# Performance work log

Hardware: AMD Instinct MI355X
Metric: run time of the kernel (lower is better)

Reference implementation:

```python
import jax, jax.numpy as jnp
import numpy as np

N, E = 50000, 800000
IN_DIM, H_DIM, OUT_DIM, EDGE_DIM, HEADS = 128, 128, 112, 8, 1
NEG_SLOPE = 0.2
BN_EPS = 1e-5


def _gat_layer(x, src, dst, edge_att, W, a_src, a_dst, We, a_edge, bias):
    """PyG GATConv (concat=False, edge_dim used for attention only)."""
    H, C = a_src.shape  # heads, out channels
    xs = (x @ W).reshape(-1, H, C)            # [N,H,C]
    ef = (edge_att @ We).reshape(-1, H, C)    # [E,H,C]
    al_src = jnp.einsum('nhc,hc->nh', xs, a_src)   # [N,H]
    al_dst = jnp.einsum('nhc,hc->nh', xs, a_dst)   # [N,H]
    al_edge = jnp.einsum('ehc,hc->eh', ef, a_edge) # [E,H]
    alpha = al_src[src] + al_dst[dst] + al_edge    # [E,H]
    alpha = jnp.where(alpha > 0, alpha, NEG_SLOPE * alpha)  # leaky_relu(0.2)
    # segment softmax over incoming edges of each dst node
    m = jax.lax.stop_gradient(jax.ops.segment_max(alpha, dst, num_segments=N))
    ex = jnp.exp(alpha - m[dst])
    den = jax.ops.segment_sum(ex, dst, num_segments=N)
    att = ex / den[dst]                       # [E,H]
    msg = xs[src] * att[:, :, None]           # [E,H,C] gather + weight
    out = jax.ops.segment_sum(msg, dst, num_segments=N)  # scatter-add [N,H,C]
    return out.mean(axis=1) + bias            # concat=False -> head mean


def _batchnorm(h, gamma, beta):
    mu = h.mean(axis=0)
    var = h.var(axis=0)
    return gamma * (h - mu) * jax.lax.rsqrt(var + BN_EPS) + beta


def setup_inputs() -> dict:
    key = jax.random.key(0)
    ks = jax.random.split(key, 20)
    s = 0.1
    inp = {
        'x': jax.random.normal(ks[0], (N, IN_DIM), dtype=jnp.float32),
        'edge_index': jax.random.randint(ks[1], (2, E), 0, N, dtype=jnp.int32),
        'edge_att': jax.random.normal(ks[2], (E, EDGE_DIM), dtype=jnp.float32),
        # layer 0: IN_DIM -> H_DIM
        'W0': s * jax.random.normal(ks[3], (IN_DIM, HEADS * H_DIM), dtype=jnp.float32),
        'a_src0': s * jax.random.normal(ks[4], (HEADS, H_DIM), dtype=jnp.float32),
        'a_dst0': s * jax.random.normal(ks[5], (HEADS, H_DIM), dtype=jnp.float32),
        'We0': s * jax.random.normal(ks[6], (EDGE_DIM, HEADS * H_DIM), dtype=jnp.float32),
        'a_edge0': s * jax.random.normal(ks[7], (HEADS, H_DIM), dtype=jnp.float32),
        'b0': jnp.zeros((H_DIM,), dtype=jnp.float32),
        # layer 1: H_DIM -> OUT_DIM
        'W1': s * jax.random.normal(ks[8], (H_DIM, HEADS * OUT_DIM), dtype=jnp.float32),
        'a_src1': s * jax.random.normal(ks[9], (HEADS, OUT_DIM), dtype=jnp.float32),
        'a_dst1': s * jax.random.normal(ks[10], (HEADS, OUT_DIM), dtype=jnp.float32),
        'We1': s * jax.random.normal(ks[11], (EDGE_DIM, HEADS * OUT_DIM), dtype=jnp.float32),
        'a_edge1': s * jax.random.normal(ks[12], (HEADS, OUT_DIM), dtype=jnp.float32),
        'b1': jnp.zeros((OUT_DIM,), dtype=jnp.float32),
        # batchnorms
        'bn_g': jnp.ones((H_DIM,), dtype=jnp.float32),
        'bn_b': jnp.zeros((H_DIM,), dtype=jnp.float32),
        'bnf_g': jnp.ones((OUT_DIM,), dtype=jnp.float32),
        'bnf_b': jnp.zeros((OUT_DIM,), dtype=jnp.float32),
    }
    return inp


def reference(x, edge_index, edge_att,
              W0, a_src0, a_dst0, We0, a_edge0, b0,
              W1, a_src1, a_dst1, We1, a_edge1, b1,
              bn_g, bn_b, bnf_g, bnf_b):
    src, dst = edge_index[0], edge_index[1]
    h = _gat_layer(x, src, dst, edge_att, W0, a_src0, a_dst0, We0, a_edge0, b0)
    h = _batchnorm(h, bn_g, bn_b)
    h = jax.nn.relu(h)
    # dropout is a no-op in eval; omitted for a deterministic reference
    h = _gat_layer(h, src, dst, edge_att, W1, a_src1, a_dst1, We1, a_edge1, b1)
    h = _batchnorm(h, bnf_g, bnf_b)
    return h
```

## Files before the change

kernel.cpp:

```cpp
#include <hip/hip_runtime.h>
#include <math.h>

#define NN 50000
#define NPAD 50048
#define NE 800000
#define SCAN_B 256
#define SCAN_NBLK ((NN + SCAN_B - 1) / SCAN_B)
#define AGG_NBLK 3200

typedef __attribute__((ext_vector_type(8))) short bf16x8;
typedef __attribute__((ext_vector_type(4))) float f32x4;
typedef __attribute__((ext_vector_type(8))) unsigned short u16x8;

__device__ __forceinline__ unsigned short f2bf(float x) {
    unsigned u = __float_as_uint(x);
    u += 0x7fffu + ((u >> 16) & 1);
    return (unsigned short)(u >> 16);
}
__device__ __forceinline__ float bf2f(unsigned short h) {
    return __uint_as_float(((unsigned)h) << 16);
}

template<int LAYER>
__device__ __forceinline__ float edge_ex(uint2 r, float aldv, const float* __restrict__ als)
{
    float ae = bf2f((unsigned short)(LAYER ? (r.y & 0xffffu) : (r.x >> 16)));
    float a = als[r.x & 0xffffu] + aldv + ae;
    a = a > 0.f ? a : 0.2f * a;
    return __expf(a);
}

__global__ void k_init_cvt(int* __restrict__ deg, float* __restrict__ stats,
                           int* __restrict__ hist, int* __restrict__ binCur,
                           const float* __restrict__ We0, const float* __restrict__ ae0,
                           const float* __restrict__ We1, const float* __restrict__ ae1,
                           float* __restrict__ ve,
                           const float* __restrict__ W0, const float* __restrict__ W1,
                           unsigned short* __restrict__ Wth0, unsigned short* __restrict__ Wtl0,
                           unsigned short* __restrict__ Wth1, unsigned short* __restrict__ Wtl1)
{
    int idx = blockIdx.x * 256 + threadIdx.x;
    if (idx < NN) deg[idx] = 0;
    if (idx < 512) stats[idx] = 0.f;
    if (idx < 64) { hist[idx] = 0; binCur[idx] = 0; }
    if (idx < 128 * 128) {
        int k = idx / 128, c = idx % 128;
        float v = W0[idx];
        unsigned short hi = f2bf(v);
        Wth0[c * 128 + k] = hi;
        Wtl0[c * 128 + k] = f2bf(v - bf2f(hi));
    } else if (idx < 128 * 128 + 128 * 112) {
        int i2 = idx - 128 * 128;
        int k = i2 / 112, c = i2 % 112;
        float v = W1[i2];
        unsigned short hi = f2bf(v);
        Wth1[c * 128 + k] = hi;
        Wtl1[c * 128 + k] = f2bf(v - bf2f(hi));
    }
    if (blockIdx.x == gridDim.x - 1) {
        int j = threadIdx.x;
        if (j < 8) {
            float s = 0.f;
            for (int c = 0; c < 128; ++c) s += We0[j * 128 + c] * ae0[c];
            ve[j] = s;
        } else if (j < 16) {
            int jj = j - 8;
            float s = 0.f;
            for (int c = 0; c < 112; ++c) s += We1[jj * 112 + c] * ae1[c];
            ve[8 + jj] = s;
        }
    }
}

__global__ void k_deg(const int* __restrict__ dst, int* __restrict__ deg,
                      int* __restrict__ rank, int E_)
{
    int i = blockIdx.x * blockDim.x + threadIdx.x;
    int e = i * 2;
    if (e + 2 <= E_) {
        int2 dd = *reinterpret_cast<const int2*>(dst + e);
        int2 rr;
        rr.x = atomicAdd(&deg[dd.x], 1);
        rr.y = atomicAdd(&deg[dd.y], 1);
        *reinterpret_cast<int2*>(rank + e) = rr;
    } else if (e < E_) {
        rank[e] = atomicAdd(&deg[dst[e]], 1);
    }
}

__global__ void k_scan1(const int* __restrict__ deg, int* __restrict__ partial,
                        int* __restrict__ hist)
{
    __shared__ int sm[SCAN_B];
    __shared__ int lh[64];
    int t = threadIdx.x;
    if (t < 64) lh[t] = 0;
    int idx = blockIdx.x * SCAN_B + t;
    int d = (idx < NN) ? deg[idx] : 0;
    sm[t] = d;
    __syncthreads();
    if (idx < NN) atomicAdd(&lh[63 - (d < 63 ? d : 63)], 1);
    #pragma unroll
    for (int off = SCAN_B / 2; off > 0; off >>= 1) {
        if (t < off) sm[t] += sm[t + off];
        __syncthreads();
    }
    if (t == 0) partial[blockIdx.x] = sm[0];
    if (t < 64 && lh[t]) atomicAdd(&hist[t], lh[t]);
}

__global__ void k_scan3(const int* __restrict__ deg, const int* __restrict__ partial,
                        int* __restrict__ rp, const int* __restrict__ hist,
                        int* __restrict__ binCur, int* __restrict__ ord)
{
    __shared__ int sm[SCAN_B];
    __shared__ int pbase;
    __shared__ int lh[64], lrsv[64], lstart[64];
    int t = threadIdx.x;
    int pv = (t < SCAN_NBLK && t < blockIdx.x) ? partial[t] : 0;
    sm[t] = pv;
    __syncthreads();
    #pragma unroll
    for (int off = SCAN_B / 2; off > 0; off >>= 1) {
        if (t < off) sm[t] += sm[t + off];
        __syncthreads();
    }
    if (t == 0) pbase = sm[0];
    __syncthreads();
    int idx = blockIdx.x * SCAN_B + t;
    int v = (idx < NN) ? deg[idx] : 0;
    sm[t] = v;
    __syncthreads();
    #pragma unroll
    for (int off = 1; off < SCAN_B; off <<= 1) {
        int u = (t >= off) ? sm[t - off] : 0;
        __syncthreads();
        sm[t] += u;
        __syncthreads();
    }
    int excl = pbase + ((t == 0) ? 0 : sm[t - 1]);
    if (idx < NN) rp[idx] = excl;
    if (idx == NN - 1) rp[NN] = excl + v;

    if (t < 64) lh[t] = 0;
    __syncthreads();
    int b = 0, lr = 0;
    if (idx < NN) {
        b = 63 - (v < 63 ? v : 63);
        lr = atomicAdd(&lh[b], 1);
    }
    __syncthreads();
    if (t < 64) {
        lrsv[t] = lh[t] ? atomicAdd(&binCur[t], lh[t]) : 0;
        int s = 0;
        for (int i = 0; i < t; ++i) s += hist[i];
        lstart[t] = s;
    }
    __syncthreads();
    if (idx < NN) ord[lstart[b] + lrsv[b] + lr] = idx;
}

__global__ void k_csr_fill(const int* __restrict__ src, const int* __restrict__ dst,
                           const float* __restrict__ eatt, const float* __restrict__ ve,
                           const int* __restrict__ rp, const int* __restrict__ rank,
                           uint2* __restrict__ pk, int E_)
{
    int i = blockIdx.x * blockDim.x + threadIdx.x;
    int e = i * 4;
    if (e >= E_) return;
    int4 ss = *reinterpret_cast<const int4*>(src + e);
    int4 dd = *reinterpret_cast<const int4*>(dst + e);
    int4 rr = *reinterpret_cast<const int4*>(rank + e);
    const float4* ea = reinterpret_cast<const float4*>(eatt + (size_t)e * 8);

    float v0 = ve[0], v1 = ve[1], v2 = ve[2], v3 = ve[3];
    float v4 = ve[4], v5 = ve[5], v6 = ve[6], v7 = ve[7];
    float w0 = ve[8], w1 = ve[9], w2 = ve[10], w3 = ve[11];
    float w4 = ve[12], w5 = ve[13], w6 = ve[14], w7 = ve[15];

    int s4[4] = {ss.x, ss.y, ss.z, ss.w};
    int d4[4] = {dd.x, dd.y, dd.z, dd.w};
    int r4[4] = {rr.x, rr.y, rr.z, rr.w};
    #pragma unroll
    for (int k = 0; k < 4; ++k) {
        float4 u0 = ea[2 * k], u1 = ea[2 * k + 1];
        float a0 = u0.x * v0 + u0.y * v1 + u0.z * v2 + u0.w * v3
                 + u1.x * v4 + u1.y * v5 + u1.z * v6 + u1.w * v7;
        float a1 = u0.x * w0 + u0.y * w1 + u0.z * w2 + u0.w * w3
                 + u1.x * w4 + u1.y * w5 + u1.z * w6 + u1.w * w7;
        int pos = rp[d4[k]] + r4[k];
        uint2 rec;
        rec.x = (unsigned)s4[k] | ((unsigned)f2bf(a0) << 16);
        rec.y = (unsigned)f2bf(a1);
        pk[pos] = rec;
    }
}

template<int COLS, bool BN_IN>
__launch_bounds__(256, 2)
__global__ void k_gemm_mfma(const void* __restrict__ A,
                            const unsigned short* __restrict__ Wth,
                            const unsigned short* __restrict__ Wtl,
                            unsigned short* __restrict__ out,
                            const float* __restrict__ a_src, const float* __restrict__ a_dst,
                            float* __restrict__ als, float* __restrict__ ald,
                            const float* __restrict__ bsum, const float* __restrict__ bsq,
                            const float* __restrict__ gamma, const float* __restrict__ beta)
{
    constexpr int NT = COLS / 16;
    __shared__ unsigned short sBh[COLS * 128];
    __shared__ unsigned short sBl[COLS * 128];
    __shared__ float scN[128], shN[128];

    int wv = threadIdx.x >> 6;
    int lane = threadIdx.x & 63;
    int r0 = blockIdx.x * 64 + wv * 16;
    int m = lane & 15;
    int quad = lane >> 4;
    int arow = r0 + m;
    int rc = (arow < NN) ? arow : NN - 1;

    float4 av[8];
    u16x8 av16[4];
    if (BN_IN) {
        const unsigned short* pa = reinterpret_cast<const unsigned short*>(A)
                                 + (size_t)rc * 128 + quad * 8;
        #pragma unroll
        for (int ks = 0; ks < 4; ++ks)
            av16[ks] = *reinterpret_cast<const u16x8*>(pa + ks * 32);
    } else {
        const float* pa = reinterpret_cast<const float*>(A) + (size_t)rc * 128 + quad * 8;
        #pragma unroll
        for (int ks = 0; ks < 4; ++ks) {
            av[2 * ks]     = *reinterpret_cast<const float4*>(pa + ks * 32);
            av[2 * ks + 1] = *reinterpret_cast<const float4*>(pa + ks * 32 + 4);
        }
    }

    constexpr int CH = COLS * 128 * 2 / 16;
    for (int i = threadIdx.x; i < CH; i += 256) {
        unsigned o = (unsigned)i * 16u;
        unsigned d = o ^ (((o >> 8) & 7u) << 4);
        *reinterpret_cast<uint4*>(reinterpret_cast<char*>(sBh) + d) =
            *reinterpret_cast<const uint4*>(reinterpret_cast<const char*>(Wth) + o);
        *reinterpret_cast<uint4*>(reinterpret_cast<char*>(sBl) + d) =
            *reinterpret_cast<const uint4*>(reinterpret_cast<const char*>(Wtl) + o);
    }
    if (BN_IN) {
        if (threadIdx.x < 128) {
            int k = threadIdx.x;
            float invn = 1.0f / (float)NN;
            float mean = bsum[k] * invn;
            float var  = bsq[k] * invn - mean * mean;
            float sc = gamma[k] * rsqrtf(var + 1e-5f);
            scN[k] = sc;
            shN[k] = beta[k] - mean * sc;
        }
    }
    __syncthreads();

    f32x4 acc[NT];
    #pragma unroll
    for (int t = 0; t < NT; ++t) acc[t] = f32x4{0.f, 0.f, 0.f, 0.f};

    unsigned swz = ((unsigned)(m & 7)) << 4;

    #pragma unroll
    for (int ks = 0; ks < 4; ++ks) {
        float vv[8];
        if (BN_IN) {
            #pragma unroll
            for (int jj = 0; jj < 8; ++jj) vv[jj] = bf2f((unsigned short)av16[ks][jj]);
        } else {
            float4 v0 = av[2 * ks], v1 = av[2 * ks + 1];
            vv[0] = v0.x; vv[1] = v0.y; vv[2] = v0.z; vv[3] = v0.w;
            vv[4] = v1.x; vv[5] = v1.y; vv[6] = v1.z; vv[7] = v1.w;
        }
        int kb = ks * 32 + quad * 8;
        bf16x8 ah, al;
        #pragma unroll
        for (int jj = 0; jj < 8; ++jj) {
            float f = vv[jj];
            if (BN_IN) f = fmaxf(f * scN[kb + jj] + shN[kb + jj], 0.f);
            unsigned short hi = f2bf(f);
            ah[jj] = (short)hi;
            al[jj] = (short)f2bf(f - bf2f(hi));
        }
        #pragma unroll
        for (int t = 0; t < NT; ++t) {
            int c = t * 16 + m;
            unsigned b = ((unsigned)c * 256u + (unsigned)ks * 64u + (unsigned)quad * 16u) ^ swz;
            bf16x8 bh = *reinterpret_cast<const bf16x8*>(reinterpret_cast<const char*>(sBh) + b);
            bf16x8 bl = *reinterpret_cast<const bf16x8*>(reinterpret_cast<const char*>(sBl) + b);
            acc[t] = __builtin_amdgcn_mfma_f32_16x16x32_bf16(ah, bh, acc[t], 0, 0, 0);
            acc[t] = __builtin_amdgcn_mfma_f32_16x16x32_bf16(al, bh, acc[t], 0, 0, 0);
            acc[t] = __builtin_amdgcn_mfma_f32_16x16x32_bf16(ah, bl, acc[t], 0, 0, 0);
        }
    }

    float p[4] = {0.f, 0.f, 0.f, 0.f}, q[4] = {0.f, 0.f, 0.f, 0.f};
    #pragma unroll
    for (int t = 0; t < NT; ++t) {
        int c = t * 16 + m;
        float asv = a_src[c], adv = a_dst[c];
        #pragma unroll
        for (int rI = 0; rI < 4; ++rI) {
            float v = acc[t][rI];
            int row = r0 + quad * 4 + rI;
            if (row < NN) out[(size_t)row * COLS + c] = f2bf(v);
            p[rI] += v * asv;
            q[rI] += v * adv;
        }
    }
    #pragma unroll
    for (int rI = 0; rI < 4; ++rI) {
        #pragma unroll
        for (int off = 1; off <= 8; off <<= 1) {
            p[rI] += __shfl_xor(p[rI], off);
            q[rI] += __shfl_xor(q[rI], off);
        }
    }
    if (m == 0) {
        #pragma unroll
        for (int rI = 0; rI < 4; ++rI) {
            int row = r0 + quad * 4 + rI;
            if (row < NN) { als[row] = p[rI]; ald[row] = q[rI]; }
        }
    }
}

template<int COLS, int LAYER>
__global__ void k_aggregate(const int* __restrict__ rp, const int* __restrict__ ord,
                            const uint2* __restrict__ pk,
                            const float* __restrict__ als, const float* __restrict__ ald,
                            const unsigned short* __restrict__ xs,
                            unsigned short* __restrict__ out,
                            float* __restrict__ psum, float* __restrict__ psq)
{
    __shared__ float sS[16 * 128], sQ[16 * 128];
    int ql = threadIdx.x & 15;
    int wq = threadIdx.x >> 4;
    int col = ql * 8;
    bool act = (col < COLS);
    int qid = blockIdx.x * 16 + wq;
    float bs[8] = {0.f,0.f,0.f,0.f,0.f,0.f,0.f,0.f};
    float bq[8] = {0.f,0.f,0.f,0.f,0.f,0.f,0.f,0.f};

    if (qid < NN) {
        int w = ord[qid];
        int beg = rp[w], end = rp[w + 1];
        float aldv = ald[w];
        float acc[8] = {0.f,0.f,0.f,0.f,0.f,0.f,0.f,0.f};
        float den = 0.f;
        int j = beg;
        for (; j + 8 <= end; j += 8) {
            uint2 r0 = pk[j],     r1 = pk[j + 1], r2 = pk[j + 2], r3 = pk[j + 3];
            uint2 r4 = pk[j + 4], r5 = pk[j + 5], r6 = pk[j + 6], r7 = pk[j + 7];
            float e0 = edge_ex<LAYER>(r0, aldv, als), e1 = edge_ex<LAYER>(r1, aldv, als);
            float e2 = edge_ex<LAYER>(r2, aldv, als), e3 = edge_ex<LAYER>(r3, aldv, als);
            float e4 = edge_ex<LAYER>(r4, aldv, als), e5 = edge_ex<LAYER>(r5, aldv, als);
            float e6 = edge_ex<LAYER>(r6, aldv, als), e7 = edge_ex<LAYER>(r7, aldv, als);
            den += ((e0 + e1) + (e2 + e3)) + ((e4 + e5) + (e6 + e7));
            if (act) {
                u16x8 u0 = *reinterpret_cast<const u16x8*>(xs + (size_t)(r0.x & 0xffffu) * COLS + col);
                u16x8 u1 = *reinterpret_cast<const u16x8*>(xs + (size_t)(r1.x & 0xffffu) * COLS + col);
                u16x8 u2 = *reinterpret_cast<const u16x8*>(xs + (size_t)(r2.x & 0xffffu) * COLS + col);
                u16x8 u3 = *reinterpret_cast<const u16x8*>(xs + (size_t)(r3.x & 0xffffu) * COLS + col);
                u16x8 u4 = *reinterpret_cast<const u16x8*>(xs + (size_t)(r4.x & 0xffffu) * COLS + col);
                u16x8 u5 = *reinterpret_cast<const u16x8*>(xs + (size_t)(r5.x & 0xffffu) * COLS + col);
                u16x8 u6 = *reinterpret_cast<const u16x8*>(xs + (size_t)(r6.x & 0xffffu) * COLS + col);
                u16x8 u7 = *reinterpret_cast<const u16x8*>(xs + (size_t)(r7.x & 0xffffu) * COLS + col);
                #pragma unroll
                for (int k = 0; k < 8; ++k)
                    acc[k] += (((e0 * bf2f(u0[k]) + e1 * bf2f(u1[k]))
                              + (e2 * bf2f(u2[k]) + e3 * bf2f(u3[k])))
                             + ((e4 * bf2f(u4[k]) + e5 * bf2f(u5[k]))
                              + (e6 * bf2f(u6[k]) + e7 * bf2f(u7[k]))));
            }
        }
        if (j < end) {
            bool v1 = j + 1 < end, v2 = j + 2 < end, v3 = j + 3 < end;
            bool v4 = j + 4 < end, v5 = j + 5 < end, v6 = j + 6 < end;
            uint2 r0 = pk[j];
            uint2 r1 = v1 ? pk[j + 1] : uint2{0u, 0u};
            uint2 r2 = v2 ? pk[j + 2] : uint2{0u, 0u};
            uint2 r3 = v3 ? pk[j + 3] : uint2{0u, 0u};
            uint2 r4 = v4 ? pk[j + 4] : uint2{0u, 0u};
            uint2 r5 = v5 ? pk[j + 5] : uint2{0u, 0u};
            uint2 r6 = v6 ? pk[j + 6] : uint2{0u, 0u};
            float e0 = edge_ex<LAYER>(r0, aldv, als);
            float e1 = v1 ? edge_ex<LAYER>(r1, aldv, als) : 0.f;
            float e2 = v2 ? edge_ex<LAYER>(r2, aldv, als) : 0.f;
            float e3 = v3 ? edge_ex<LAYER>(r3, aldv, als) : 0.f;
            float e4 = v4 ? edge_ex<LAYER>(r4, aldv, als) : 0.f;
            float e5 = v5 ? edge_ex<LAYER>(r5, aldv, als) : 0.f;
            float e6 = v6 ? edge_ex<LAYER>(r6, aldv, als) : 0.f;
            den += ((e0 + e1) + (e2 + e3)) + ((e4 + e5) + e6);
            if (act) {
                u16x8 u0 = *reinterpret_cast<const u16x8*>(xs + (size_t)(r0.x & 0xffffu) * COLS + col);
                #pragma unroll
                for (int k = 0; k < 8; ++k) acc[k] += e0 * bf2f(u0[k]);
                if (v1) {
                    u16x8 u = *reinterpret_cast<const u16x8*>(xs + (size_t)(r1.x & 0xffffu) * COLS + col);
                    #pragma unroll
                    for (int k = 0; k < 8; ++k) acc[k] += e1 * bf2f(u[k]);
                }
                if (v2) {
                    u16x8 u = *reinterpret_cast<const u16x8*>(xs + (size_t)(r2.x & 0xffffu) * COLS + col);
                    #pragma unroll
                    for (int k = 0; k < 8; ++k) acc[k] += e2 * bf2f(u[k]);
                }
                if (v3) {
                    u16x8 u = *reinterpret_cast<const u16x8*>(xs + (size_t)(r3.x & 0xffffu) * COLS + col);
                    #pragma unroll
                    for (int k = 0; k < 8; ++k) acc[k] += e3 * bf2f(u[k]);
                }
                if (v4) {
                    u16x8 u = *reinterpret_cast<const u16x8*>(xs + (size_t)(r4.x & 0xffffu) * COLS + col);
                    #pragma unroll
                    for (int k = 0; k < 8; ++k) acc[k] += e4 * bf2f(u[k]);
                }
                if (v5) {
                    u16x8 u = *reinterpret_cast<const u16x8*>(xs + (size_t)(r5.x & 0xffffu) * COLS + col);
                    #pragma unroll
                    for (int k = 0; k < 8; ++k) acc[k] += e5 * bf2f(u[k]);
                }
                if (v6) {
                    u16x8 u = *reinterpret_cast<const u16x8*>(xs + (size_t)(r6.x & 0xffffu) * COLS + col);
                    #pragma unroll
                    for (int k = 0; k < 8; ++k) acc[k] += e6 * bf2f(u[k]);
                }
            }
        }
        float inv = (end > beg) ? 1.f / den : 0.f;
        if (act) {
            float o[8];
            u16x8 ob;
            #pragma unroll
            for (int k = 0; k < 8; ++k) {
                o[k] = acc[k] * inv;
                bs[k] += o[k];
                bq[k] += o[k] * o[k];
                ob[k] = f2bf(o[k]);
            }
            __builtin_nontemporal_store(ob,
                reinterpret_cast<u16x8*>(out + (size_t)w * COLS + col));
        }
    }
    #pragma unroll
    for (int k = 0; k < 8; ++k) {
        sS[wq * 128 + col + k] = act ? bs[k] : 0.f;
        sQ[wq * 128 + col + k] = act ? bq[k] : 0.f;
    }
    __syncthreads();
    int t = threadIdx.x;
    if (t < 128) {
        float s = 0.f, s2 = 0.f;
        #pragma unroll
        for (int r = 0; r < 16; ++r) { s += sS[r * 128 + t]; s2 += sQ[r * 128 + t]; }
        psum[(size_t)blockIdx.x * 128 + t] = s;
        psq [(size_t)blockIdx.x * 128 + t] = s2;
    }
}

__global__ void k_bn_stats2(const float* __restrict__ psum, const float* __restrict__ psq,
                            float* __restrict__ sums, float* __restrict__ sqs)
{
    int t = threadIdx.x;
    int c = t & 127;
    constexpr int ROWS = AGG_NBLK / 128;
    const float* sp = (t < 128) ? psum : psq;
    float s = 0.f;
    #pragma unroll 5
    for (int i = 0; i < ROWS; ++i)
        s += sp[(size_t)(blockIdx.x * ROWS + i) * 128 + c];
    unsafeAtomicAdd(((t < 128) ? sums : sqs) + c, s);
}

template<int COLS>
__global__ void k_bn_apply(const unsigned short* __restrict__ in, float* __restrict__ out,
                           const float* __restrict__ sums, const float* __restrict__ sqs,
                           const float* __restrict__ gamma, const float* __restrict__ beta,
                           int n)
{
    int idx = blockIdx.x * blockDim.x + threadIdx.x;
    if (idx >= n * COLS) return;
    int c = idx % COLS;
    float invn = 1.0f / (float)n;
    float mean = sums[c] * invn;
    float var  = sqs[c] * invn - mean * mean;
    float sc = gamma[c] * rsqrtf(var + 1e-5f);
    float sh = beta[c] - mean * sc;
    out[idx] = bf2f(in[idx]) * sc + sh;
}

extern "C" void kernel_launch(void* const* d_in, const int* in_sizes, int n_in,
                              void* d_out, int out_size, void* d_ws, size_t ws_size,
                              hipStream_t stream)
{
    const float* x    = (const float*)d_in[0];
    const int*   eidx = (const int*)d_in[1];
    const float* eatt = (const float*)d_in[2];
    const float* W0   = (const float*)d_in[3];
    const float* as0  = (const float*)d_in[4];
    const float* ad0  = (const float*)d_in[5];
    const float* We0  = (const float*)d_in[6];
    const float* ae0  = (const float*)d_in[7];
    const float* W1   = (const float*)d_in[9];
    const float* as1  = (const float*)d_in[10];
    const float* ad1  = (const float*)d_in[11];
    const float* We1  = (const float*)d_in[12];
    const float* ae1  = (const float*)d_in[13];
    const float* bng  = (const float*)d_in[15];
    const float* bnb  = (const float*)d_in[16];
    const float* bnfg = (const float*)d_in[17];
    const float* bnfb = (const float*)d_in[18];

    const int N = NN, E = NE;
    const int* src = eidx;
    const int* dst = eidx + E;

    float* ws = (float*)d_ws;
    size_t off = 0;
    unsigned short* xs0b = (unsigned short*)(ws + off); off += (size_t)N * 64;
    unsigned short* h = (unsigned short*)(ws + off);    off += (size_t)N * 64;
    unsigned short* xs1b = (unsigned short*)(ws + off); off += (size_t)N * 56;
    uint2* pk = (uint2*)(ws + off);     off += (size_t)E * 2;
    int*   rp   = (int*)(ws + off);     off += N + 2;
    int*   ord  = (int*)(ws + off);     off += N;
    float* als0 = ws + off;     off += N;
    float* ald0 = ws + off;     off += N;
    float* als1 = ws + off;     off += N;
    float* ald1 = ws + off;     off += N;
    float* stats = ws + off;    off += 512;
    float* ve = ws + off;       off += 16;
    int*   hist = (int*)(ws + off);     off += 64;
    int*   binCur = (int*)(ws + off);   off += 64;
    int*   partial = (int*)(ws + off);  off += SCAN_NBLK;
    float* psum = ws + off;     off += (size_t)AGG_NBLK * 128;
    float* psq  = ws + off;     off += (size_t)AGG_NBLK * 128;
    unsigned short* Wth0 = (unsigned short*)(ws + off); off += 128 * 64;
    unsigned short* Wtl0 = (unsigned short*)(ws + off); off += 128 * 64;
    unsigned short* Wth1 = (unsigned short*)(ws + off); off += 112 * 64;
    unsigned short* Wtl1 = (unsigned short*)(ws + off); off += 112 * 64;

    int*   rank = (int*)h;
    int*   deg  = ((int*)h) + 800000;
    unsigned short* out1 = h;

    float* sum0 = stats;
    float* sq0  = stats + 128;
    float* sum1 = stats + 256;
    float* sq1  = stats + 384;

    k_init_cvt<<<(N + 255) / 256, 256, 0, stream>>>(deg, stats, hist, binCur,
                                                    We0, ae0, We1, ae1, ve,
                                                    W0, W1, Wth0, Wtl0, Wth1, Wtl1);

    k_deg<<<(E / 2 + 255) / 256, 256, 0, stream>>>(dst, deg, rank, E);
    k_scan1<<<SCAN_NBLK, SCAN_B, 0, stream>>>(deg, partial, hist);
    k_scan3<<<SCAN_NBLK, SCAN_B, 0, stream>>>(deg, partial, rp, hist, binCur, ord);
    k_csr_fill<<<(E / 4 + 255) / 256, 256, 0, stream>>>(src, dst, eatt, ve, rp, rank, pk, E);

    k_gemm_mfma<128, false><<<NPAD / 64, 256, 0, stream>>>(x, Wth0, Wtl0, xs0b,
                                                           as0, ad0, als0, ald0,
                                                           nullptr, nullptr, nullptr, nullptr);
    k_aggregate<128, 0><<<AGG_NBLK, 256, 0, stream>>>(rp, ord, pk, als0, ald0, xs0b, h, psum, psq);
    k_bn_stats2<<<128, 256, 0, stream>>>(psum, psq, sum0, sq0);

    k_gemm_mfma<112, true><<<NPAD / 64, 256, 0, stream>>>(h, Wth1, Wtl1, xs1b,
                                                          as1, ad1, als1, ald1,
                                                          sum0, sq0, bng, bnb);
    k_aggregate<112, 1><<<AGG_NBLK, 256, 0, stream>>>(rp, ord, pk, als1, ald1, xs1b, out1, psum, psq);
    k_bn_stats2<<<128, 256, 0, stream>>>(psum, psq, sum1, sq1);
    k_bn_apply<112><<<(N * 112 + 255) / 256, 256, 0, stream>>>(out1, (float*)d_out, sum1, sq1, bnfg, bnfb, N);
}
```

Before: 329.4 us.

## Build CSR via two-pass bucketed scatter and pack row ranges into order array

Replaces per-edge rank atomics with a coarse bucket scatter (atomic per 49-node bucket) into a temp buffer, followed by a per-bucket local placement pass using shared-memory counters. The node order array now carries row begin/end so aggregation skips separate rp lookups. BN apply is vectorised to four elements per thread. The extra pass and contended bucket counters trade against better write locality and removing the rank array.

```diff
diff --git a/kernel.cpp b/kernel.cpp
--- a/kernel.cpp
+++ b/kernel.cpp
@@ -7,6 +7,8 @@
 #define SCAN_B 256
 #define SCAN_NBLK ((NN + SCAN_B - 1) / SCAN_B)
 #define AGG_NBLK 3200
+#define NBUCK 1024
+#define BWID 49
 
 typedef __attribute__((ext_vector_type(8))) short bf16x8;
 typedef __attribute__((ext_vector_type(4))) float f32x4;
@@ -72,19 +74,18 @@
     }
 }
 
-__global__ void k_deg(const int* __restrict__ dst, int* __restrict__ deg,
-                      int* __restrict__ rank, int E_)
+__global__ void k_deg(const int* __restrict__ dst, int* __restrict__ deg, int E_)
 {
     int i = blockIdx.x * blockDim.x + threadIdx.x;
-    int e = i * 2;
-    if (e + 2 <= E_) {
-        int2 dd = *reinterpret_cast<const int2*>(dst + e);
-        int2 rr;
-        rr.x = atomicAdd(&deg[dd.x], 1);
-        rr.y = atomicAdd(&deg[dd.y], 1);
-        *reinterpret_cast<int2*>(rank + e) = rr;
-    } else if (e < E_) {
-        rank[e] = atomicAdd(&deg[dst[e]], 1);
+    int e = i * 4;
+    if (e + 4 <= E_) {
+        int4 dd = *reinterpret_cast<const int4*>(dst + e);
+        atomicAdd(&deg[dd.x], 1);
+        atomicAdd(&deg[dd.y], 1);
+        atomicAdd(&deg[dd.z], 1);
+        atomicAdd(&deg[dd.w], 1);
+    } else {
+        for (; e < E_; ++e) atomicAdd(&deg[dst[e]], 1);
     }
 }
 
@@ -111,7 +112,7 @@
 
 __global__ void k_scan3(const int* __restrict__ deg, const int* __restrict__ partial,
                         int* __restrict__ rp, const int* __restrict__ hist,
-                        int* __restrict__ binCur, int* __restrict__ ord)
+                        int* __restrict__ binCur, uint4* __restrict__ ordq)
 {
     __shared__ int sm[SCAN_B];
     __shared__ int pbase;
@@ -157,20 +158,34 @@
         lstart[t] = s;
     }
     __syncthreads();
-    if (idx < NN) ord[lstart[b] + lrsv[b] + lr] = idx;
-}
-
-__global__ void k_csr_fill(const int* __restrict__ src, const int* __restrict__ dst,
-                           const float* __restrict__ eatt, const float* __restrict__ ve,
-                           const int* __restrict__ rp, const int* __restrict__ rank,
-                           uint2* __restrict__ pk, int E_)
+    if (idx < NN) {
+        uint4 rec;
+        rec.x = (unsigned)idx;
+        rec.y = (unsigned)excl;
+        rec.z = (unsigned)(excl + v);
+        rec.w = 0u;
+        ordq[lstart[b] + lrsv[b] + lr] = rec;
+    }
+}
+
+__global__ void k_binit(const int* __restrict__ rp, int* __restrict__ bcur)
+{
+    int b = blockIdx.x * blockDim.x + threadIdx.x;
+    if (b < NBUCK) {
+        int nb = b * BWID;
+        bcur[b] = rp[nb < NN ? nb : NN];
+    }
+}
+
+__global__ void k_fill_p1(const int* __restrict__ src, const int* __restrict__ dst,
+                          const float* __restrict__ eatt, const float* __restrict__ ve,
+                          int* __restrict__ bcur, uint2* __restrict__ tmp, int E_)
 {
     int i = blockIdx.x * blockDim.x + threadIdx.x;
     int e = i * 4;
     if (e >= E_) return;
     int4 ss = *reinterpret_cast<const int4*>(src + e);
     int4 dd = *reinterpret_cast<const int4*>(dst + e);
-    int4 rr = *reinterpret_cast<const int4*>(rank + e);
     const float4* ea = reinterpret_cast<const float4*>(eatt + (size_t)e * 8);
 
     float v0 = ve[0], v1 = ve[1], v2 = ve[2], v3 = ve[3];
@@ -180,7 +195,6 @@
 
     int s4[4] = {ss.x, ss.y, ss.z, ss.w};
     int d4[4] = {dd.x, dd.y, dd.z, dd.w};
-    int r4[4] = {rr.x, rr.y, rr.z, rr.w};
     #pragma unroll
     for (int k = 0; k < 4; ++k) {
         float4 u0 = ea[2 * k], u1 = ea[2 * k + 1];
@@ -188,11 +202,36 @@
                  + u1.x * v4 + u1.y * v5 + u1.z * v6 + u1.w * v7;
         float a1 = u0.x * w0 + u0.y * w1 + u0.z * w2 + u0.w * w3
                  + u1.x * w4 + u1.y * w5 + u1.z * w6 + u1.w * w7;
-        int pos = rp[d4[k]] + r4[k];
+        int d = d4[k];
+        int pos = atomicAdd(&bcur[d / BWID], 1);
         uint2 rec;
         rec.x = (unsigned)s4[k] | ((unsigned)f2bf(a0) << 16);
-        rec.y = (unsigned)f2bf(a1);
-        pk[pos] = rec;
+        rec.y = (unsigned)d     | ((unsigned)f2bf(a1) << 16);
+        tmp[pos] = rec;
+    }
+}
+
+__global__ void k_fill_p2(const int* __restrict__ rp, const uint2* __restrict__ tmp,
+                          uint2* __restrict__ pk)
+{
+    __shared__ int lcnt[BWID];
+    int b = blockIdx.x;
+    int t = threadIdx.x;
+    int nb0 = b * BWID;
+    int nb1 = nb0 + BWID;
+    int beg = rp[nb0 < NN ? nb0 : NN];
+    int end = rp[nb1 < NN ? nb1 : NN];
+    if (t < BWID) lcnt[t] = 0;
+    __syncthreads();
+    for (int i = beg + t; i < end; i += 256) {
+        uint2 r = tmp[i];
+        int d = (int)(r.y & 0xffffu);
+        int lr = atomicAdd(&lcnt[d - nb0], 1);
+        int pos = rp[d] + lr;
+        uint2 o;
+        o.x = r.x;
+        o.y = r.y >> 16;
+        pk[pos] = o;
     }
 }
 
@@ -330,8 +369,7 @@
 }
 
 template<int COLS, int LAYER>
-__global__ void k_aggregate(const int* __restrict__ rp, const int* __restrict__ ord,
-                            const uint2* __restrict__ pk,
+__global__ void k_aggregate(const uint4* __restrict__ ordq, const uint2* __restrict__ pk,
                             const float* __restrict__ als, const float* __restrict__ ald,
                             const unsigned short* __restrict__ xs,
                             unsigned short* __restrict__ out,
@@ -347,8 +385,9 @@
     float bq[8] = {0.f,0.f,0.f,0.f,0.f,0.f,0.f,0.f};
 
     if (qid < NN) {
-        int w = ord[qid];
-        int beg = rp[w], end = rp[w + 1];
+        uint4 o4 = ordq[qid];
+        int w = (int)o4.x;
+        int beg = (int)o4.y, end = (int)o4.z;
         float aldv = ald[w];
         float acc[8] = {0.f,0.f,0.f,0.f,0.f,0.f,0.f,0.f};
         float den = 0.f;
@@ -483,15 +522,26 @@
                            const float* __restrict__ gamma, const float* __restrict__ beta,
                            int n)
 {
-    int idx = blockIdx.x * blockDim.x + threadIdx.x;
-    if (idx >= n * COLS) return;
-    int c = idx % COLS;
+    int g = blockIdx.x * blockDim.x + threadIdx.x;
+    int base = g * 4;
+    if (base >= n * COLS) return;
+    int c0 = base % COLS;
+    ushort4 v = *reinterpret_cast<const ushort4*>(in + base);
     float invn = 1.0f / (float)n;
-    float mean = sums[c] * invn;
-    float var  = sqs[c] * invn - mean * mean;
-    float sc = gamma[c] * rsqrtf(var + 1e-5f);
-    float sh = beta[c] - mean * sc;
-    out[idx] = bf2f(in[idx]) * sc + sh;
+    float4 o;
+    unsigned short vv[4] = {v.x, v.y, v.z, v.w};
+    float oo[4];
+    #pragma unroll
+    for (int k = 0; k < 4; ++k) {
+        int c = c0 + k;
+        float mean = sums[c] * invn;
+        float var  = sqs[c] * invn - mean * mean;
+        float sc = gamma[c] * rsqrtf(var + 1e-5f);
+        float sh = beta[c] - mean * sc;
+        oo[k] = bf2f(vv[k]) * sc + sh;
+    }
+    o.x = oo[0]; o.y = oo[1]; o.z = oo[2]; o.w = oo[3];
+    *reinterpret_cast<float4*>(out + base) = o;
 }
 
 extern "C" void kernel_launch(void* const* d_in, const int* in_sizes, int n_in,
@@ -527,7 +577,8 @@
     unsigned short* xs1b = (unsigned short*)(ws + off); off += (size_t)N * 56;
     uint2* pk = (uint2*)(ws + off);     off += (size_t)E * 2;
     int*   rp   = (int*)(ws + off);     off += N + 2;
-    int*   ord  = (int*)(ws + off);     off += N;
+    uint4* ordq = (uint4*)(ws + off);   off += (size_t)N * 4;
+    int*   deg  = (int*)(ws + off);     off += N;
     float* als0 = ws + off;     off += N;
     float* ald0 = ws + off;     off += N;
     float* als1 = ws + off;     off += N;
@@ -536,6 +587,7 @@
     float* ve = ws + off;       off += 16;
     int*   hist = (int*)(ws + off);     off += 64;
     int*   binCur = (int*)(ws + off);   off += 64;
+    int*   bcur = (int*)(ws + off);     off += NBUCK;
     int*   partial = (int*)(ws + off);  off += SCAN_NBLK;
     float* psum = ws + off;     off += (size_t)AGG_NBLK * 128;
     float* psq  = ws + off;     off += (size_t)AGG_NBLK * 128;
@@ -544,8 +596,7 @@
     unsigned short* Wth1 = (unsigned short*)(ws + off); off += 112 * 64;
     unsigned short* Wtl1 = (unsigned short*)(ws + off); off += 112 * 64;
 
-    int*   rank = (int*)h;
-    int*   deg  = ((int*)h) + 800000;
+    uint2* tmp = (uint2*)xs1b;
     unsigned short* out1 = h;
 
     float* sum0 = stats;
@@ -557,21 +608,23 @@
                                                     We0, ae0, We1, ae1, ve,
                                                     W0, W1, Wth0, Wtl0, Wth1, Wtl1);
 
-    k_deg<<<(E / 2 + 255) / 256, 256, 0, stream>>>(dst, deg, rank, E);
+    k_deg<<<(E / 4 + 255) / 256, 256, 0, stream>>>(dst, deg, E);
     k_scan1<<<SCAN_NBLK, SCAN_B, 0, stream>>>(deg, partial, hist);
-    k_scan3<<<SCAN_NBLK, SCAN_B, 0, stream>>>(deg, partial, rp, hist, binCur, ord);
-    k_csr_fill<<<(E / 4 + 255) / 256, 256, 0, stream>>>(src, dst, eatt, ve, rp, rank, pk, E);
+    k_scan3<<<SCAN_NBLK, SCAN_B, 0, stream>>>(deg, partial, rp, hist, binCur, ordq);
+    k_binit<<<(NBUCK + 255) / 256, 256, 0, stream>>>(rp, bcur);
+    k_fill_p1<<<(E / 4 + 255) / 256, 256, 0, stream>>>(src, dst, eatt, ve, bcur, tmp, E);
+    k_fill_p2<<<NBUCK, 256, 0, stream>>>(rp, tmp, pk);
 
     k_gemm_mfma<128, false><<<NPAD / 64, 256, 0, stream>>>(x, Wth0, Wtl0, xs0b,
                                                            as0, ad0, als0, ald0,
                                                            nullptr, nullptr, nullptr, nullptr);
-    k_aggregate<128, 0><<<AGG_NBLK, 256, 0, stream>>>(rp, ord, pk, als0, ald0, xs0b, h, psum, psq);
+    k_aggregate<128, 0><<<AGG_NBLK, 256, 0, stream>>>(ordq, pk, als0, ald0, xs0b, h, psum, psq);
     k_bn_stats2<<<128, 256, 0, stream>>>(psum, psq, sum0, sq0);
 
     k_gemm_mfma<112, true><<<NPAD / 64, 256, 0, stream>>>(h, Wth1, Wtl1, xs1b,
                                                           as1, ad1, als1, ald1,
                                                           sum0, sq0, bng, bnb);
-    k_aggregate<112, 1><<<AGG_NBLK, 256, 0, stream>>>(rp, ord, pk, als1, ald1, xs1b, out1, psum, psq);
+    k_aggregate<112, 1><<<AGG_NBLK, 256, 0, stream>>>(ordq, pk, als1, ald1, xs1b, out1, psum, psq);
     k_bn_stats2<<<128, 256, 0, stream>>>(psum, psq, sum1, sq1);
-    k_bn_apply<112><<<(N * 112 + 255) / 256, 256, 0, stream>>>(out1, (float*)d_out, sum1, sq1, bnfg, bnfb, N);
-}
+    k_bn_apply<112><<<(N * 112 / 4 + 255) / 256, 256, 0, stream>>>(out1, (float*)d_out, sum1, sq1, bnfg, bnfb, N);
+}
```

Result: slower. 465.9 us (+41.4%).
